# Kernel tuning notes

Hardware: AMD Instinct MI355X
Metric: run time of the kernel (lower is better)

Reference implementation:

```python
import jax, jax.numpy as jnp
import numpy as np
import math

# LLaMA-7B-style int8 attention (torch-int Int8LlamaAttention)
B, S, HID, NH, HD = 2, 1024, 4096, 32, 128
THETA = 10000.0
# per-tensor quantization scales (as produced by from_float)
S_IN, S_W, S_B = 0.02, 0.01, 0.1
S_Q, S_K, S_V, S_O = 0.05, 0.05, 0.05, 0.05


def _rope_tables(position_ids):
    inv_freq = 1.0 / (THETA ** (jnp.arange(0, HD, 2, dtype=jnp.float32) / HD))
    freqs = position_ids.astype(jnp.float32)[..., None] * inv_freq  # [B,S,HD//2]
    emb = jnp.concatenate([freqs, freqs], axis=-1)  # [B,S,HD]
    return jnp.cos(emb)[:, None], jnp.sin(emb)[:, None]  # [B,1,S,HD]


def _rotate_half(x):
    return jnp.concatenate([-x[..., HD // 2:], x[..., :HD // 2]], axis=-1)


def _quant_i8(x):
    return jnp.clip(jnp.round(x), -128, 127).astype(jnp.int8)


def _w8a8b8o8(x_i8, w_i8, b_i8, alpha, beta):
    # int8 GEMM with int32 accumulation, fused dequant-requant to int8
    acc = jnp.einsum('bsk,nk->bsn', x_i8.astype(jnp.int32), w_i8.astype(jnp.int32))
    return _quant_i8(acc.astype(jnp.float32) * alpha + b_i8.astype(jnp.float32) * beta)


def setup_inputs() -> dict:
    key = jax.random.key(0)
    ks = jax.random.split(key, 9)
    ri8 = lambda k, shp: jax.random.randint(k, shp, -127, 128, dtype=jnp.int8)
    return {
        'hidden_states': jax.random.normal(ks[0], (B, S, HID), jnp.float32),
        'position_ids': jnp.broadcast_to(jnp.arange(S, dtype=jnp.int32), (B, S)),
        'w_q': ri8(ks[1], (HID, HID)),
        'w_k': ri8(ks[2], (HID, HID)),
        'w_v': ri8(ks[3], (HID, HID)),
        'w_o': ri8(ks[4], (HID, HID)),
        'b_q': ri8(ks[5], (HID,)),
        'b_k': ri8(ks[6], (HID,)),
        'b_v': ri8(ks[7], (HID,)),
        'b_o': jax.random.normal(ks[8], (HID,), jnp.float32) * 0.01,
    }


def reference(hidden_states, position_ids, w_q, w_k, w_v, w_o, b_q, b_k, b_v, b_o):
    # quantize activations, run int8 q/k/v projections (W8A8B8O8Linear)
    x_i8 = _quant_i8(hidden_states / S_IN)
    q = _w8a8b8o8(x_i8, w_q, b_q, S_IN * S_W / S_Q, S_B / S_Q)
    k = _w8a8b8o8(x_i8, w_k, b_k, S_IN * S_W / S_K, S_B / S_K)
    v = _w8a8b8o8(x_i8, w_v, b_v, S_IN * S_W / S_V, S_B / S_V)
    to_heads = lambda t: t.reshape(B, S, NH, HD).transpose(0, 2, 1, 3)  # [B,NH,S,HD]
    q, k, v = to_heads(q), to_heads(k), to_heads(v)
    # RoPE applied on dequantized int8 values, requantized for the int8 qk bmm
    cos, sin = _rope_tables(position_ids)
    qf, kf = q.astype(jnp.float32), k.astype(jnp.float32)
    q_i8 = _quant_i8(qf * cos + _rotate_half(qf) * sin)
    k_i8 = _quant_i8(kf * cos + _rotate_half(kf) * sin)
    # BMM_S8T_S8N_F32T: int8 QK^T -> fp32 with scale s_q*s_k, then /sqrt(d)
    attn = jnp.einsum('bhsd,bhtd->bhst', q_i8.astype(jnp.int32), k_i8.astype(jnp.int32))
    attn = attn.astype(jnp.float32) * (S_Q * S_K) / math.sqrt(HD)
    # NOTE: source never applies the attention mask (`attn_weights = attn_weights`)
    p = jax.nn.softmax(attn, axis=-1)
    # probs quantized to int8 with scale 1/127 for BMM_S8T_S8N_S8T
    p_i8 = _quant_i8(p * 127.0)
    ctx = jnp.einsum('bhst,bhtd->bhsd', p_i8.astype(jnp.int32), v.astype(jnp.int32))
    ctx_i8 = _quant_i8(ctx.astype(jnp.float32) * ((1.0 / 127.0) * S_V / S_O))
    ctx_i8 = ctx_i8.transpose(0, 2, 1, 3).reshape(B, S, HID)
    # W8A8BFP32OFP32 o_proj: int8 GEMM, fp32 output + fp32 bias
    out = jnp.einsum('bsk,nk->bsn', ctx_i8.astype(jnp.int32), w_o.astype(jnp.int32))
    return out.astype(jnp.float32) * (S_O * S_W) + b_o
```

## Files before the change

kernel.cpp:

```cpp
#include <hip/hip_runtime.h>
#include <hip/hip_bf16.h>
#include <cstdint>
#include <cstddef>

typedef int v4i __attribute__((ext_vector_type(4)));

#define NH 32
#define HD 128
#define SEQ 1024
#define HID 4096
#define BB 2
#define BKB 128

__device__ __forceinline__ signed char quant_i8(float x) {
    float r = rintf(x);
    r = fminf(fmaxf(r, -128.0f), 127.0f);
    return (signed char)r;
}

#define GLOAD_LDS16(g, l) \
    __builtin_amdgcn_global_load_lds((const __attribute__((address_space(1))) void*)(g), \
                                     (__attribute__((address_space(3))) void*)(l), 16, 0, 0)

__global__ __launch_bounds__(256) void pack4_i8_kernel(
    const int* __restrict__ s0, const int* __restrict__ s1,
    const int* __restrict__ s2, const int* __restrict__ s3,
    signed char* __restrict__ d0, signed char* __restrict__ d1,
    signed char* __restrict__ d2, signed char* __restrict__ d3, int n4)
{
    int i = blockIdx.x * 256 + threadIdx.x;
    int which = i >> 22;
    int idx = i & ((1 << 22) - 1);
    const int* src = (which == 0) ? s0 : (which == 1) ? s1 : (which == 2) ? s2 : s3;
    signed char* dst = (which == 0) ? d0 : (which == 1) ? d1 : (which == 2) ? d2 : d3;
    int4 v = ((const int4*)src)[idx];
    char4 c;
    c.x = (signed char)v.x; c.y = (signed char)v.y;
    c.z = (signed char)v.z; c.w = (signed char)v.w;
    ((char4*)dst)[idx] = c;
}

__global__ __launch_bounds__(256) void quant_x_kernel(const float* __restrict__ src,
                                                      signed char* __restrict__ dst, int n4) {
    int i = blockIdx.x * 256 + threadIdx.x;
    if (i >= n4) return;
    float4 v = ((const float4*)src)[i];
    char4 c;
    c.x = quant_i8(v.x * 50.0f);
    c.y = quant_i8(v.y * 50.0f);
    c.z = quant_i8(v.z * 50.0f);
    c.w = quant_i8(v.w * 50.0f);
    ((char4*)dst)[i] = c;
}

template<bool F32OUT>
__device__ __forceinline__ void gemm_core_db(
    const signed char* __restrict__ A, const signed char* __restrict__ Bw,
    const void* __restrict__ bias, void* __restrict__ outp,
    int m0, int n0, int N, int K, float alpha, float beta)
{
    __shared__ __align__(16) signed char sA[2 * 128 * BKB];
    __shared__ __align__(16) signed char sB[2 * 128 * BKB];

    const int t    = threadIdx.x;
    const int w    = t >> 6;
    const int lane = t & 63;
    const int lm   = lane & 15;
    const int quad = lane >> 4;
    const int wm   = (w >> 1) * 64;
    const int wn   = (w & 1) * 64;

    int srow[4], skc[4];
    #pragma unroll
    for (int p = 0; p < 4; p++) {
        int si = t + 256 * p;
        int row = si >> 3;
        srow[p] = row;
        skc[p] = ((si & 7) - row) & 7;
    }

    v4i acc[4][4] = {};

    #pragma unroll
    for (int p = 0; p < 4; p++) {
        GLOAD_LDS16(A  + (size_t)(m0 + srow[p]) * K + skc[p] * 16, sA + t * 16 + p * 4096);
        GLOAD_LDS16(Bw + (size_t)(n0 + srow[p]) * K + skc[p] * 16, sB + t * 16 + p * 4096);
    }

    int buf = 0;
    for (int k0 = 0; k0 < K; k0 += BKB) {
        __syncthreads();

        if (k0 + BKB < K) {
            int nb = buf ^ 1;
            #pragma unroll
            for (int p = 0; p < 4; p++) {
                GLOAD_LDS16(A  + (size_t)(m0 + srow[p]) * K + k0 + BKB + skc[p] * 16,
                            sA + nb * 16384 + t * 16 + p * 4096);
                GLOAD_LDS16(Bw + (size_t)(n0 + srow[p]) * K + k0 + BKB + skc[p] * 16,
                            sB + nb * 16384 + t * 16 + p * 4096);
            }
        }

        const signed char* pA = sA + buf * 16384;
        const signed char* pB = sB + buf * 16384;
        #pragma unroll
        for (int ks = 0; ks < 2; ks++) {
            const int slot = (ks * 4 + quad + lm) & 7;
            v4i af[4], bf[4];
            #pragma unroll
            for (int i = 0; i < 4; i++) {
                int row = wm + 16 * i + lm;
                af[i] = *(const v4i*)(pA + row * BKB + slot * 16);
            }
            #pragma unroll
            for (int j = 0; j < 4; j++) {
                int row = wn + 16 * j + lm;
                bf[j] = *(const v4i*)(pB + row * BKB + slot * 16);
            }
            #pragma unroll
            for (int i = 0; i < 4; i++)
                #pragma unroll
                for (int j = 0; j < 4; j++)
                    acc[i][j] = __builtin_amdgcn_mfma_i32_16x16x64_i8(af[i], bf[j], acc[i][j], 0, 0, 0);
        }
        buf ^= 1;
    }

    const int orow = quad * 4;
    #pragma unroll
    for (int i = 0; i < 4; i++) {
        #pragma unroll
        for (int j = 0; j < 4; j++) {
            #pragma unroll
            for (int r = 0; r < 4; r++) {
                int row = m0 + wm + 16 * i + orow + r;
                int col = n0 + wn + 16 * j + lm;
                float v = (float)acc[i][j][r];
                if (F32OUT) {
                    ((float*)outp)[(size_t)row * N + col] = v * alpha + ((const float*)bias)[col];
                } else {
                    float q = v * alpha + (float)((const int*)bias)[col] * beta;
                    ((signed char*)outp)[(size_t)row * N + col] = quant_i8(q);
                }
            }
        }
    }
}

__global__ __launch_bounds__(256) void gemm_qkv(
    const signed char* __restrict__ x8,
    const signed char* __restrict__ wq, const signed char* __restrict__ wk,
    const signed char* __restrict__ wv,
    const int* __restrict__ bq, const int* __restrict__ bk, const int* __restrict__ bv,
    signed char* __restrict__ q8, signed char* __restrict__ k8, signed char* __restrict__ v8)
{
    const int id  = blockIdx.x + 96 * blockIdx.y;
    const int xcd = id & 7;
    const int j   = id >> 3;
    const int g   = j >> 6;
    const int r   = j & 63;
    const int nb  = xcd * 12 + g * 4 + (r & 3);
    const int m0  = (r >> 2) * 128;
    const int which = nb >> 5;
    const int n0  = (nb & 31) * 128;
    const signed char* Bw = (which == 0) ? wq : (which == 1) ? wk : wv;
    const int* bias = (which == 0) ? bq : (which == 1) ? bk : bv;
    signed char* outp = (which == 0) ? q8 : (which == 1) ? k8 : v8;
    gemm_core_db<false>(x8, Bw, bias, outp, m0, n0, HID, HID, 0.004f, 2.0f);
}

__global__ __launch_bounds__(256) void gemm_o(
    const signed char* __restrict__ c8, const signed char* __restrict__ wo,
    const float* __restrict__ bo, float* __restrict__ outp)
{
    const int id  = blockIdx.x + 32 * blockIdx.y;
    const int xcd = id & 7;
    const int j   = id >> 3;
    const int nb  = xcd * 4 + (j & 3);
    const int m0  = (j >> 2) * 128;
    gemm_core_db<true>(c8, wo, bo, outp, m0, nb * 128, HID, HID, 0.0005f, 0.0f);
}

__global__ __launch_bounds__(128) void rope_kernel(
    const int* __restrict__ pos_ids, signed char* __restrict__ q,
    signed char* __restrict__ k, const signed char* __restrict__ v,
    signed char* __restrict__ vt)
{
    const int bid = blockIdx.x;
    const int sg = bid & 127;
    const int h  = (bid >> 7) & (NH - 1);
    const int b  = bid >> 12;
    const int d  = threadIdx.x;
    const int s0 = sg * 8;
    const int bh = b * NH + h;

    float inv = expf(-(float)(2 * (d & 63)) * (9.210340371976184f / 128.0f));

    float qd[8], qp[8], kd[8], kp[8];
    signed char vd[8];
    int pos[8];
    size_t base[8];
    #pragma unroll
    for (int i = 0; i < 8; i++) {
        int s = s0 + i;
        base[i] = ((size_t)(b * SEQ + s) * NH + h) * (size_t)HD;
        pos[i] = pos_ids[b * SEQ + s];
        qd[i] = (float)q[base[i] + d];
        qp[i] = (float)q[base[i] + (d ^ 64)];
        kd[i] = (float)k[base[i] + d];
        kp[i] = (float)k[base[i] + (d ^ 64)];
        vd[i] = v[base[i] + d];
    }
    __syncthreads();

    union { signed char c[8]; int2 i2; } vu;
    #pragma unroll
    for (int i = 0; i < 8; i++) {
        float freq = (float)pos[i] * inv;
        float cs, sn;
        __sincosf(freq, &sn, &cs);
        float rotq = (d < 64) ? -qp[i] : qp[i];
        float rotk = (d < 64) ? -kp[i] : kp[i];
        q[base[i] + d] = quant_i8(qd[i] * cs + rotq * sn);
        k[base[i] + d] = quant_i8(kd[i] * cs + rotk * sn);
        vu.c[i] = vd[i];
    }
    *(int2*)(vt + ((size_t)(bh * HD + d)) * SEQ + s0) = vu.i2;
}

__global__ __launch_bounds__(256) void attn_kernel(
    const signed char* __restrict__ q, const signed char* __restrict__ k,
    const signed char* __restrict__ vt, signed char* __restrict__ ctx)
{
    __shared__ __align__(16) signed char p8[32 * 1040];
    __shared__ float red[128];

    const int w    = threadIdx.x >> 6;
    const int lane = threadIdx.x & 63;
    const int bid  = blockIdx.x;
    const int mt   = bid & 31;
    const int bh   = bid >> 5;
    const int b    = bh >> 5, h = bh & 31;
    const int m0   = mt * 32;
    const int lm   = lane & 15;
    const int quad = lane >> 4;

    const float SCALE = 0.0025f / 11.313708498984761f;
    const float LOG2E = 1.4426950408889634f;

    const signed char* qb_base = q + ((size_t)(b * SEQ + m0 + lm) * NH + h) * (size_t)HD + quad * 16;
    v4i qb0 = *(const v4i*)qb_base;
    v4i qb1 = *(const v4i*)(qb_base + 64);
    const signed char* qb_base2 = qb_base + (size_t)16 * NH * HD;
    v4i qb2 = *(const v4i*)qb_base2;
    v4i qb3 = *(const v4i*)(qb_base2 + 64);

    float vals0[16][4], vals1[16][4];
    #pragma unroll
    for (int j = 0; j < 16; j++) {
        int t0 = w * 256 + j * 16;
        const signed char* kb = k + ((size_t)(b * SEQ + t0 + lm) * NH + h) * (size_t)HD + quad * 16;
        v4i a0 = *(const v4i*)kb;
        v4i a1 = *(const v4i*)(kb + 64);
        v4i acc0 = {}, acc1 = {};
        __builtin_amdgcn_s_setprio(1);
        acc0 = __builtin_amdgcn_mfma_i32_16x16x64_i8(a0, qb0, acc0, 0, 0, 0);
        acc0 = __builtin_amdgcn_mfma_i32_16x16x64_i8(a1, qb1, acc0, 0, 0, 0);
        acc1 = __builtin_amdgcn_mfma_i32_16x16x64_i8(a0, qb2, acc1, 0, 0, 0);
        acc1 = __builtin_amdgcn_mfma_i32_16x16x64_i8(a1, qb3, acc1, 0, 0, 0);
        __builtin_amdgcn_s_setprio(0);
        #pragma unroll
        for (int r = 0; r < 4; r++) {
            vals0[j][r] = (float)acc0[r] * SCALE;
            vals1[j][r] = (float)acc1[r] * SCALE;
        }
    }

    float mx0 = vals0[0][0], mx1 = vals1[0][0];
    #pragma unroll
    for (int j = 0; j < 16; j++)
        #pragma unroll
        for (int r = 0; r < 4; r++) {
            mx0 = fmaxf(mx0, vals0[j][r]);
            mx1 = fmaxf(mx1, vals1[j][r]);
        }
    mx0 = fmaxf(mx0, __shfl_xor(mx0, 16)); mx0 = fmaxf(mx0, __shfl_xor(mx0, 32));
    mx1 = fmaxf(mx1, __shfl_xor(mx1, 16)); mx1 = fmaxf(mx1, __shfl_xor(mx1, 32));
    if (lane < 16) { red[w * 16 + lane] = mx0; red[64 + w * 16 + lane] = mx1; }
    __syncthreads();
    mx0 = fmaxf(fmaxf(red[lm], red[16 + lm]), fmaxf(red[32 + lm], red[48 + lm]));
    mx1 = fmaxf(fmaxf(red[64 + lm], red[80 + lm]), fmaxf(red[96 + lm], red[112 + lm]));

    float sum0 = 0.f, sum1 = 0.f;
    #pragma unroll
    for (int j = 0; j < 16; j++)
        #pragma unroll
        for (int r = 0; r < 4; r++) {
            vals0[j][r] = exp2f((vals0[j][r] - mx0) * LOG2E); sum0 += vals0[j][r];
            vals1[j][r] = exp2f((vals1[j][r] - mx1) * LOG2E); sum1 += vals1[j][r];
        }
    sum0 += __shfl_xor(sum0, 16); sum0 += __shfl_xor(sum0, 32);
    sum1 += __shfl_xor(sum1, 16); sum1 += __shfl_xor(sum1, 32);
    __syncthreads();
    if (lane < 16) { red[w * 16 + lane] = sum0; red[64 + w * 16 + lane] = sum1; }
    __syncthreads();
    sum0 = (red[lm] + red[16 + lm]) + (red[32 + lm] + red[48 + lm]);
    sum1 = (red[64 + lm] + red[80 + lm]) + (red[96 + lm] + red[112 + lm]);
    float sf0 = 127.0f / sum0, sf1 = 127.0f / sum1;

    #pragma unroll
    for (int j = 0; j < 16; j++) {
        union { signed char cc[4]; int ii; } u0, u1;
        #pragma unroll
        for (int r = 0; r < 4; r++) {
            u0.cc[r] = quant_i8(vals0[j][r] * sf0);
            u1.cc[r] = quant_i8(vals1[j][r] * sf1);
        }
        int ch = (((w * 16 + j) + 4 * lm) & 63) * 16 + quad * 4;
        *(int*)(p8 + lm * 1040 + ch) = u0.ii;
        *(int*)(p8 + (16 + lm) * 1040 + ch) = u1.ii;
    }
    __syncthreads();

    v4i accp0[2] = {}, accp1[2] = {};
    for (int kk = 0; kk < SEQ; kk += 64) {
        int ph = (((kk >> 4) + quad) + 4 * lm) & 63;
        v4i af0 = *(const v4i*)(p8 + lm * 1040 + ph * 16);
        v4i af1 = *(const v4i*)(p8 + (16 + lm) * 1040 + ph * 16);
        v4i vb0 = *(const v4i*)(vt + ((size_t)(bh * HD + w * 32 + lm)) * (size_t)SEQ + kk + quad * 16);
        v4i vb1 = *(const v4i*)(vt + ((size_t)(bh * HD + w * 32 + 16 + lm)) * (size_t)SEQ + kk + quad * 16);
        __builtin_amdgcn_s_setprio(1);
        accp0[0] = __builtin_amdgcn_mfma_i32_16x16x64_i8(af0, vb0, accp0[0], 0, 0, 0);
        accp1[0] = __builtin_amdgcn_mfma_i32_16x16x64_i8(af1, vb0, accp1[0], 0, 0, 0);
        accp0[1] = __builtin_amdgcn_mfma_i32_16x16x64_i8(af0, vb1, accp0[1], 0, 0, 0);
        accp1[1] = __builtin_amdgcn_mfma_i32_16x16x64_i8(af1, vb1, accp1[1], 0, 0, 0);
        __builtin_amdgcn_s_setprio(0);
    }
    #pragma unroll
    for (int j = 0; j < 2; j++) {
        #pragma unroll
        for (int r = 0; r < 4; r++) {
            int row = quad * 4 + r;
            int col = w * 32 + j * 16 + lm;
            ctx[((size_t)(b * SEQ + m0 + row) * NH + h) * (size_t)HD + col] =
                quant_i8((float)accp0[j][r] * (1.0f / 127.0f));
            ctx[((size_t)(b * SEQ + m0 + 16 + row) * NH + h) * (size_t)HD + col] =
                quant_i8((float)accp1[j][r] * (1.0f / 127.0f));
        }
    }
}

extern "C" void kernel_launch(void* const* d_in, const int* in_sizes, int n_in,
                              void* d_out, int out_size, void* d_ws, size_t ws_size,
                              hipStream_t stream)
{
    const float* hidden = (const float*)d_in[0];
    const int* pos_ids  = (const int*)d_in[1];
    const int* w_q = (const int*)d_in[2];
    const int* w_k = (const int*)d_in[3];
    const int* w_v = (const int*)d_in[4];
    const int* w_o = (const int*)d_in[5];
    const int* b_q = (const int*)d_in[6];
    const int* b_k = (const int*)d_in[7];
    const int* b_v = (const int*)d_in[8];
    const float* b_o = (const float*)d_in[9];
    float* out = (float*)d_out;

    char* ws = (char*)d_ws;
    const size_t WSZ = (size_t)HID * HID;
    signed char* wq8 = (signed char*)ws;
    signed char* wk8 = wq8 + WSZ;
    signed char* wv8 = wk8 + WSZ;
    signed char* wo8 = wv8 + WSZ;
    signed char* x8  = wo8 + WSZ;
    const size_t ASZ = (size_t)BB * SEQ * HID;
    signed char* q8  = x8 + ASZ;
    signed char* k8  = q8 + ASZ;
    signed char* v8  = k8 + ASZ;
    signed char* vt8 = v8 + ASZ;
    signed char* c8  = vt8 + ASZ;

    int wn4 = HID * HID / 4;
    pack4_i8_kernel<<<4 * wn4 / 256, 256, 0, stream>>>(w_q, w_k, w_v, w_o,
                                                       wq8, wk8, wv8, wo8, wn4);
    int xn4 = (int)(ASZ / 4);
    quant_x_kernel<<<xn4 / 256, 256, 0, stream>>>(hidden, x8, xn4);

    gemm_qkv<<<dim3(96, 16), 256, 0, stream>>>(x8, wq8, wk8, wv8, b_q, b_k, b_v,
                                               q8, k8, v8);

    rope_kernel<<<BB * NH * (SEQ / 8), 128, 0, stream>>>(pos_ids, q8, k8, v8, vt8);
    attn_kernel<<<BB * NH * (SEQ / 32), 256, 0, stream>>>(q8, k8, vt8, c8);

    gemm_o<<<dim3(32, 16), 256, 0, stream>>>(c8, wo8, b_o, out);
}
```

Measured before the change: 549.3 us.

## Rewrite int8 GEMMs with larger 512-thread tiles and 4-stage pipelined LDS loads

Replaces the double-buffered 128x128 int8 GEMM core with a templated kernel that uses 256-wide N tiles (256x256 for QKV, 128x256 for O), 512 threads and a 4-slot LDS ring with BK=64. Loads are prefetched two k-steps ahead, with explicit vmcnt waits, raw barriers and setprio around the MFMA bursts. The aim is better global-load/compute overlap and more data reuse per tile, at the cost of dropping the XCD-aware block swizzle and adding fragile hand-tuned wait counts.

Measured after the change: 558.6 us. About the same (+1.7%).

```diff
diff --git a/kernel.cpp b/kernel.cpp
--- a/kernel.cpp
+++ b/kernel.cpp
@@ -10,7 +10,6 @@
 #define SEQ 1024
 #define HID 4096
 #define BB 2
-#define BKB 128
 
 __device__ __forceinline__ signed char quant_i8(float x) {
     float r = rintf(x);
@@ -53,83 +52,110 @@
     ((char4*)dst)[i] = c;
 }
 
-template<bool F32OUT>
-__device__ __forceinline__ void gemm_core_db(
+template<int MFRAG, bool F32OUT>
+__device__ __forceinline__ void gemm8p(
     const signed char* __restrict__ A, const signed char* __restrict__ Bw,
     const void* __restrict__ bias, void* __restrict__ outp,
     int m0, int n0, int N, int K, float alpha, float beta)
 {
-    __shared__ __align__(16) signed char sA[2 * 128 * BKB];
-    __shared__ __align__(16) signed char sB[2 * 128 * BKB];
+    constexpr int BM = MFRAG * 32;
+    constexpr int BN = 256;
+    constexpr int LA = BM / 128;
+    constexpr int LB = BN / 128;
+    const int NKT = K >> 6;
+
+    __shared__ __align__(16) signed char sA[4][BM * 64];
+    __shared__ __align__(16) signed char sB[4][BN * 64];
 
     const int t    = threadIdx.x;
     const int w    = t >> 6;
     const int lane = t & 63;
     const int lm   = lane & 15;
     const int quad = lane >> 4;
-    const int wm   = (w >> 1) * 64;
-    const int wn   = (w & 1) * 64;
-
-    int srow[4], skc[4];
-    #pragma unroll
-    for (int p = 0; p < 4; p++) {
-        int si = t + 256 * p;
-        int row = si >> 3;
-        srow[p] = row;
-        skc[p] = ((si & 7) - row) & 7;
-    }
-
-    v4i acc[4][4] = {};
-
-    #pragma unroll
-    for (int p = 0; p < 4; p++) {
-        GLOAD_LDS16(A  + (size_t)(m0 + srow[p]) * K + skc[p] * 16, sA + t * 16 + p * 4096);
-        GLOAD_LDS16(Bw + (size_t)(n0 + srow[p]) * K + skc[p] * 16, sB + t * 16 + p * 4096);
-    }
-
-    int buf = 0;
-    for (int k0 = 0; k0 < K; k0 += BKB) {
-        __syncthreads();
-
-        if (k0 + BKB < K) {
-            int nb = buf ^ 1;
+    const int wm   = (w >> 2) * (BM / 2);
+    const int wn   = (w & 3) * 64;
+
+    v4i acc[MFRAG][4] = {};
+
+    auto stageA = [&](int kt) {
+        const signed char* src = A + (size_t)m0 * K + (kt << 6);
+        signed char* dst = &sA[kt & 3][0];
+        #pragma unroll
+        for (int p = 0; p < LA; p++) {
+            int si = p * 512 + t;
+            int row = si >> 2;
+            int c = ((si & 3) - (row >> 1)) & 3;
+            GLOAD_LDS16(src + (size_t)row * K + c * 16, dst + si * 16);
+        }
+    };
+    auto stageB = [&](int kt) {
+        const signed char* src = Bw + (size_t)n0 * K + (kt << 6);
+        signed char* dst = &sB[kt & 3][0];
+        #pragma unroll
+        for (int p = 0; p < LB; p++) {
+            int si = p * 512 + t;
+            int row = si >> 2;
+            int c = ((si & 3) - (row >> 1)) & 3;
+            GLOAD_LDS16(src + (size_t)row * K + c * 16, dst + si * 16);
+        }
+    };
+    auto rd = [&](const signed char* p, int rowl) -> v4i {
+        return *(const v4i*)(p + rowl * 64 + ((((rowl >> 1) + quad) & 3) << 4));
+    };
+
+    stageA(0); stageB(0);
+    stageA(1); stageB(1);
+    if constexpr (LA + LB == 4) asm volatile("s_waitcnt vmcnt(4)" ::: "memory");
+    else                        asm volatile("s_waitcnt vmcnt(3)" ::: "memory");
+    __builtin_amdgcn_s_barrier();
+
+    for (int kt = 0; kt < NKT; kt++) {
+        const signed char* pA = &sA[kt & 3][0];
+        const signed char* pB = &sB[kt & 3][0];
+        const bool pre = (kt + 2 < NKT);
+
+        v4i bf[4], af[4];
+        #pragma unroll
+        for (int j = 0; j < 4; j++) bf[j] = rd(pB, wn + 16 * j + lm);
+        #pragma unroll
+        for (int i = 0; i < 4; i++) af[i] = rd(pA, wm + 16 * i + lm);
+        if (pre) stageA(kt + 2);
+        if constexpr (MFRAG == 4) {
+            if (pre) stageB(kt + 2);
+            if (kt < NKT - 2)       asm volatile("s_waitcnt vmcnt(3)" ::: "memory");
+            else if (kt == NKT - 2) asm volatile("s_waitcnt vmcnt(0)" ::: "memory");
+        }
+        __builtin_amdgcn_s_barrier();
+        __builtin_amdgcn_s_setprio(1);
+        #pragma unroll
+        for (int i = 0; i < 4; i++)
             #pragma unroll
-            for (int p = 0; p < 4; p++) {
-                GLOAD_LDS16(A  + (size_t)(m0 + srow[p]) * K + k0 + BKB + skc[p] * 16,
-                            sA + nb * 16384 + t * 16 + p * 4096);
-                GLOAD_LDS16(Bw + (size_t)(n0 + srow[p]) * K + k0 + BKB + skc[p] * 16,
-                            sB + nb * 16384 + t * 16 + p * 4096);
-            }
-        }
-
-        const signed char* pA = sA + buf * 16384;
-        const signed char* pB = sB + buf * 16384;
-        #pragma unroll
-        for (int ks = 0; ks < 2; ks++) {
-            const int slot = (ks * 4 + quad + lm) & 7;
-            v4i af[4], bf[4];
+            for (int j = 0; j < 4; j++)
+                acc[i][j] = __builtin_amdgcn_mfma_i32_16x16x64_i8(af[i], bf[j], acc[i][j], 0, 0, 0);
+        __builtin_amdgcn_s_setprio(0);
+        __builtin_amdgcn_s_barrier();
+
+        if constexpr (MFRAG == 8) {
             #pragma unroll
-            for (int i = 0; i < 4; i++) {
-                int row = wm + 16 * i + lm;
-                af[i] = *(const v4i*)(pA + row * BKB + slot * 16);
-            }
-            #pragma unroll
-            for (int j = 0; j < 4; j++) {
-                int row = wn + 16 * j + lm;
-                bf[j] = *(const v4i*)(pB + row * BKB + slot * 16);
-            }
+            for (int i = 0; i < 4; i++) af[i] = rd(pA, wm + 64 + 16 * i + lm);
+            if (pre) stageB(kt + 2);
+            if (kt < NKT - 2)       asm volatile("s_waitcnt vmcnt(4)" ::: "memory");
+            else if (kt == NKT - 2) asm volatile("s_waitcnt vmcnt(0)" ::: "memory");
+            __builtin_amdgcn_s_barrier();
+            __builtin_amdgcn_s_setprio(1);
             #pragma unroll
             for (int i = 0; i < 4; i++)
                 #pragma unroll
                 for (int j = 0; j < 4; j++)
-                    acc[i][j] = __builtin_amdgcn_mfma_i32_16x16x64_i8(af[i], bf[j], acc[i][j], 0, 0, 0);
-        }
-        buf ^= 1;
+                    acc[4 + i][j] = __builtin_amdgcn_mfma_i32_16x16x64_i8(af[i], bf[j], acc[4 + i][j], 0, 0, 0);
+            __builtin_amdgcn_s_setprio(0);
+            __builtin_amdgcn_s_barrier();
+        }
     }
 
     const int orow = quad * 4;
     #pragma unroll
-    for (int i = 0; i < 4; i++) {
+    for (int i = 0; i < MFRAG; i++) {
         #pragma unroll
         for (int j = 0; j < 4; j++) {
             #pragma unroll
@@ -148,38 +174,31 @@
     }
 }
 
-__global__ __launch_bounds__(256) void gemm_qkv(
+__global__ __launch_bounds__(512, 2) void gemm_qkv(
     const signed char* __restrict__ x8,
     const signed char* __restrict__ wq, const signed char* __restrict__ wk,
     const signed char* __restrict__ wv,
     const int* __restrict__ bq, const int* __restrict__ bk, const int* __restrict__ bv,
     signed char* __restrict__ q8, signed char* __restrict__ k8, signed char* __restrict__ v8)
 {
-    const int id  = blockIdx.x + 96 * blockIdx.y;
-    const int xcd = id & 7;
-    const int j   = id >> 3;
-    const int g   = j >> 6;
-    const int r   = j & 63;
-    const int nb  = xcd * 12 + g * 4 + (r & 3);
-    const int m0  = (r >> 2) * 128;
-    const int which = nb >> 5;
-    const int n0  = (nb & 31) * 128;
+    const int id = blockIdx.x;
+    const int nb = id % 48;
+    const int mt = id / 48;
+    const int which = nb >> 4;
+    const int n0 = (nb & 15) * 256;
     const signed char* Bw = (which == 0) ? wq : (which == 1) ? wk : wv;
     const int* bias = (which == 0) ? bq : (which == 1) ? bk : bv;
     signed char* outp = (which == 0) ? q8 : (which == 1) ? k8 : v8;
-    gemm_core_db<false>(x8, Bw, bias, outp, m0, n0, HID, HID, 0.004f, 2.0f);
-}
-
-__global__ __launch_bounds__(256) void gemm_o(
+    gemm8p<8, false>(x8, Bw, bias, outp, mt * 256, n0, HID, HID, 0.004f, 2.0f);
+}
+
+__global__ __launch_bounds__(512, 2) void gemm_o(
     const signed char* __restrict__ c8, const signed char* __restrict__ wo,
     const float* __restrict__ bo, float* __restrict__ outp)
 {
-    const int id  = blockIdx.x + 32 * blockIdx.y;
-    const int xcd = id & 7;
-    const int j   = id >> 3;
-    const int nb  = xcd * 4 + (j & 3);
-    const int m0  = (j >> 2) * 128;
-    gemm_core_db<true>(c8, wo, bo, outp, m0, nb * 128, HID, HID, 0.0005f, 0.0f);
+    const int id = blockIdx.x;
+    gemm8p<4, true>(c8, wo, bo, outp, (id >> 4) * 128, (id & 15) * 256,
+                    HID, HID, 0.0005f, 0.0f);
 }
 
 __global__ __launch_bounds__(128) void rope_kernel(
@@ -387,11 +406,11 @@
     int xn4 = (int)(ASZ / 4);
     quant_x_kernel<<<xn4 / 256, 256, 0, stream>>>(hidden, x8, xn4);
 
-    gemm_qkv<<<dim3(96, 16), 256, 0, stream>>>(x8, wq8, wk8, wv8, b_q, b_k, b_v,
-                                               q8, k8, v8);
+    gemm_qkv<<<384, 512, 0, stream>>>(x8, wq8, wk8, wv8, b_q, b_k, b_v,
+                                      q8, k8, v8);
 
     rope_kernel<<<BB * NH * (SEQ / 8), 128, 0, stream>>>(pos_ids, q8, k8, v8, vt8);
     attn_kernel<<<BB * NH * (SEQ / 32), 256, 0, stream>>>(q8, k8, vt8, c8);
 
-    gemm_o<<<dim3(32, 16), 256, 0, stream>>>(c8, wo8, b_o, out);
-}
+    gemm_o<<<256, 512, 0, stream>>>(c8, wo8, b_o, out);
+}
```

## Prepack weights in MFMA fragment order and load B directly to registers

Applied to the files above, without the earlier changes.

The weight pack kernel now writes int8 weights in MFMA fragment order, so each lane can load its B fragment from global memory straight into registers without staging through LDS. The GEMM tile becomes 128x256 with BK=64, and only A goes through LDS with two buffers and explicit waitcnt/barrier pipelining plus setprio around the MFMA bursts. Grids are flattened with XCD-aware tile mapping and launch bounds ask for 2 blocks per CU. The aim is to cut LDS traffic and LDS usage for B and raise reuse per block, at the cost of more registers (32 accumulators) and reliance on hand-tuned vmcnt counts.

New measurement: 987.2 us. +79.7%, slower.

```diff
diff --git a/kernel.cpp b/kernel.cpp
--- a/kernel.cpp
+++ b/kernel.cpp
@@ -10,7 +10,6 @@
 #define SEQ 1024
 #define HID 4096
 #define BB 2
-#define BKB 128
 
 __device__ __forceinline__ signed char quant_i8(float x) {
     float r = rintf(x);
@@ -22,22 +21,32 @@
     __builtin_amdgcn_global_load_lds((const __attribute__((address_space(1))) void*)(g), \
                                      (__attribute__((address_space(3))) void*)(l), 16, 0, 0)
 
-__global__ __launch_bounds__(256) void pack4_i8_kernel(
+__global__ __launch_bounds__(256) void pack_frag_kernel(
     const int* __restrict__ s0, const int* __restrict__ s1,
     const int* __restrict__ s2, const int* __restrict__ s3,
     signed char* __restrict__ d0, signed char* __restrict__ d1,
-    signed char* __restrict__ d2, signed char* __restrict__ d3, int n4)
-{
-    int i = blockIdx.x * 256 + threadIdx.x;
-    int which = i >> 22;
-    int idx = i & ((1 << 22) - 1);
+    signed char* __restrict__ d2, signed char* __restrict__ d3)
+{
+    int g = blockIdx.x * 256 + threadIdx.x;
+    int which = g >> 20;
+    int u = g & 0xFFFFF;
+    int n  = u >> 8;
+    int kc = u & 255;
     const int* src = (which == 0) ? s0 : (which == 1) ? s1 : (which == 2) ? s2 : s3;
     signed char* dst = (which == 0) ? d0 : (which == 1) ? d1 : (which == 2) ? d2 : d3;
-    int4 v = ((const int4*)src)[idx];
-    char4 c;
-    c.x = (signed char)v.x; c.y = (signed char)v.y;
-    c.z = (signed char)v.z; c.w = (signed char)v.w;
-    ((char4*)dst)[idx] = c;
+
+    const int4* sp = (const int4*)(src + (size_t)n * HID + kc * 16);
+    union { signed char c[16]; int4 v; } out;
+    #pragma unroll
+    for (int q = 0; q < 4; q++) {
+        int4 v = sp[q];
+        out.c[4 * q + 0] = (signed char)v.x;
+        out.c[4 * q + 1] = (signed char)v.y;
+        out.c[4 * q + 2] = (signed char)v.z;
+        out.c[4 * q + 3] = (signed char)v.w;
+    }
+    int nf = n >> 4, kt = kc >> 2, ln = (kc & 3) * 16 + (n & 15);
+    ((int4*)dst)[(size_t)(nf * 64 + kt) * 64 + ln] = out.v;
 }
 
 __global__ __launch_bounds__(256) void quant_x_kernel(const float* __restrict__ src,
@@ -54,88 +63,108 @@
 }
 
 template<bool F32OUT>
-__device__ __forceinline__ void gemm_core_db(
-    const signed char* __restrict__ A, const signed char* __restrict__ Bw,
+__device__ __forceinline__ void gemm_dfb(
+    const signed char* __restrict__ A,
+    const signed char* __restrict__ Bp,
     const void* __restrict__ bias, void* __restrict__ outp,
     int m0, int n0, int N, int K, float alpha, float beta)
 {
-    __shared__ __align__(16) signed char sA[2 * 128 * BKB];
-    __shared__ __align__(16) signed char sB[2 * 128 * BKB];
+    __shared__ __align__(16) signed char sA0[128 * 64];
+    __shared__ __align__(16) signed char sA1[128 * 64];
 
     const int t    = threadIdx.x;
     const int w    = t >> 6;
     const int lane = t & 63;
     const int lm   = lane & 15;
     const int quad = lane >> 4;
-    const int wm   = (w >> 1) * 64;
-    const int wn   = (w & 1) * 64;
-
-    int srow[4], skc[4];
-    #pragma unroll
-    for (int p = 0; p < 4; p++) {
-        int si = t + 256 * p;
-        int row = si >> 3;
-        srow[p] = row;
-        skc[p] = ((si & 7) - row) & 7;
-    }
-
-    v4i acc[4][4] = {};
-
-    #pragma unroll
-    for (int p = 0; p < 4; p++) {
-        GLOAD_LDS16(A  + (size_t)(m0 + srow[p]) * K + skc[p] * 16, sA + t * 16 + p * 4096);
-        GLOAD_LDS16(Bw + (size_t)(n0 + srow[p]) * K + skc[p] * 16, sB + t * 16 + p * 4096);
-    }
-
-    int buf = 0;
-    for (int k0 = 0; k0 < K; k0 += BKB) {
-        __syncthreads();
-
-        if (k0 + BKB < K) {
-            int nb = buf ^ 1;
+    const int KT   = K >> 6;
+
+    const int r0 = t >> 2,          c0 = ((t & 3) - r0) & 3;
+    const int r1 = (t + 256) >> 2,  c1 = (((t + 256) & 3) - r1) & 3;
+    const signed char* aSrc0 = A + (size_t)(m0 + r0) * K + c0 * 16;
+    const signed char* aSrc1 = A + (size_t)(m0 + r1) * K + c1 * 16;
+
+    const size_t jstride = (size_t)KT * 1024;
+    const signed char* bBase = Bp + (size_t)((n0 >> 4) + w * 4) * jstride + (size_t)lane * 16;
+
+    v4i acc[8][4] = {};
+    v4i bfA[4], bfB[4], af[8];
+
+    auto stageA = [&](signed char* dst, int kt) {
+        GLOAD_LDS16(aSrc0 + kt * 64, dst + t * 16);
+        GLOAD_LDS16(aSrc1 + kt * 64, dst + (t + 256) * 16);
+    };
+    auto loadB = [&](v4i* bf, int kt) {
+        const signed char* p = bBase + (size_t)kt * 1024;
+        #pragma unroll
+        for (int j = 0; j < 4; j++) bf[j] = *(const v4i*)(p + (size_t)j * jstride);
+    };
+    auto rdA = [&](const signed char* slot) {
+        #pragma unroll
+        for (int i = 0; i < 8; i++) {
+            int r = 16 * i + lm;
+            af[i] = *(const v4i*)(slot + r * 64 + (((r + quad) & 3) << 4));
+        }
+    };
+
+    stageA(sA0, 0);
+    __builtin_amdgcn_sched_barrier(0);
+    loadB(bfA, 0);
+    asm volatile("s_waitcnt vmcnt(4)" ::: "memory");
+    __builtin_amdgcn_s_barrier();
+
+    for (int kt = 0; kt < KT; kt += 2) {
+        stageA(sA1, kt + 1);
+        __builtin_amdgcn_sched_barrier(0);
+        loadB(bfB, kt + 1);
+        __builtin_amdgcn_sched_barrier(0);
+        rdA(sA0);
+        __builtin_amdgcn_s_setprio(1);
+        #pragma unroll
+        for (int i = 0; i < 8; i++)
             #pragma unroll
-            for (int p = 0; p < 4; p++) {
-                GLOAD_LDS16(A  + (size_t)(m0 + srow[p]) * K + k0 + BKB + skc[p] * 16,
-                            sA + nb * 16384 + t * 16 + p * 4096);
-                GLOAD_LDS16(Bw + (size_t)(n0 + srow[p]) * K + k0 + BKB + skc[p] * 16,
-                            sB + nb * 16384 + t * 16 + p * 4096);
-            }
-        }
-
-        const signed char* pA = sA + buf * 16384;
-        const signed char* pB = sB + buf * 16384;
-        #pragma unroll
-        for (int ks = 0; ks < 2; ks++) {
-            const int slot = (ks * 4 + quad + lm) & 7;
-            v4i af[4], bf[4];
+            for (int j = 0; j < 4; j++)
+                acc[i][j] = __builtin_amdgcn_mfma_i32_16x16x64_i8(af[i], bfA[j], acc[i][j], 0, 0, 0);
+        __builtin_amdgcn_s_setprio(0);
+        asm volatile("s_waitcnt vmcnt(4)" ::: "memory");
+        __builtin_amdgcn_s_barrier();
+
+        if (kt + 2 < KT) {
+            stageA(sA0, kt + 2);
+            __builtin_amdgcn_sched_barrier(0);
+            loadB(bfA, kt + 2);
+            __builtin_amdgcn_sched_barrier(0);
+            rdA(sA1);
+            __builtin_amdgcn_s_setprio(1);
             #pragma unroll
-            for (int i = 0; i < 4; i++) {
-                int row = wm + 16 * i + lm;
-                af[i] = *(const v4i*)(pA + row * BKB + slot * 16);
-            }
-            #pragma unroll
-            for (int j = 0; j < 4; j++) {
-                int row = wn + 16 * j + lm;
-                bf[j] = *(const v4i*)(pB + row * BKB + slot * 16);
-            }
-            #pragma unroll
-            for (int i = 0; i < 4; i++)
+            for (int i = 0; i < 8; i++)
                 #pragma unroll
                 for (int j = 0; j < 4; j++)
-                    acc[i][j] = __builtin_amdgcn_mfma_i32_16x16x64_i8(af[i], bf[j], acc[i][j], 0, 0, 0);
-        }
-        buf ^= 1;
+                    acc[i][j] = __builtin_amdgcn_mfma_i32_16x16x64_i8(af[i], bfB[j], acc[i][j], 0, 0, 0);
+            __builtin_amdgcn_s_setprio(0);
+            asm volatile("s_waitcnt vmcnt(4)" ::: "memory");
+            __builtin_amdgcn_s_barrier();
+        } else {
+            rdA(sA1);
+            __builtin_amdgcn_s_setprio(1);
+            #pragma unroll
+            for (int i = 0; i < 8; i++)
+                #pragma unroll
+                for (int j = 0; j < 4; j++)
+                    acc[i][j] = __builtin_amdgcn_mfma_i32_16x16x64_i8(af[i], bfB[j], acc[i][j], 0, 0, 0);
+            __builtin_amdgcn_s_setprio(0);
+        }
     }
 
     const int orow = quad * 4;
     #pragma unroll
-    for (int i = 0; i < 4; i++) {
+    for (int i = 0; i < 8; i++) {
         #pragma unroll
         for (int j = 0; j < 4; j++) {
             #pragma unroll
             for (int r = 0; r < 4; r++) {
-                int row = m0 + wm + 16 * i + orow + r;
-                int col = n0 + wn + 16 * j + lm;
+                int row = m0 + 16 * i + orow + r;
+                int col = n0 + w * 64 + 16 * j + lm;
                 float v = (float)acc[i][j][r];
                 if (F32OUT) {
                     ((float*)outp)[(size_t)row * N + col] = v * alpha + ((const float*)bias)[col];
@@ -148,38 +177,36 @@
     }
 }
 
-__global__ __launch_bounds__(256) void gemm_qkv(
+__global__ __launch_bounds__(256, 2) void gemm_qkv(
     const signed char* __restrict__ x8,
     const signed char* __restrict__ wq, const signed char* __restrict__ wk,
     const signed char* __restrict__ wv,
     const int* __restrict__ bq, const int* __restrict__ bk, const int* __restrict__ bv,
     signed char* __restrict__ q8, signed char* __restrict__ k8, signed char* __restrict__ v8)
 {
-    const int id  = blockIdx.x + 96 * blockIdx.y;
+    const int id  = blockIdx.x;
     const int xcd = id & 7;
     const int j   = id >> 3;
-    const int g   = j >> 6;
-    const int r   = j & 63;
-    const int nb  = xcd * 12 + g * 4 + (r & 3);
-    const int m0  = (r >> 2) * 128;
-    const int which = nb >> 5;
-    const int n0  = (nb & 31) * 128;
+    const int nb  = xcd * 6 + (j >> 4);
+    const int mt  = j & 15;
+    const int which = nb >> 4;
+    const int n0  = (nb & 15) * 256;
     const signed char* Bw = (which == 0) ? wq : (which == 1) ? wk : wv;
     const int* bias = (which == 0) ? bq : (which == 1) ? bk : bv;
     signed char* outp = (which == 0) ? q8 : (which == 1) ? k8 : v8;
-    gemm_core_db<false>(x8, Bw, bias, outp, m0, n0, HID, HID, 0.004f, 2.0f);
-}
-
-__global__ __launch_bounds__(256) void gemm_o(
+    gemm_dfb<false>(x8, Bw, bias, outp, mt * 128, n0, HID, HID, 0.004f, 2.0f);
+}
+
+__global__ __launch_bounds__(256, 2) void gemm_o(
     const signed char* __restrict__ c8, const signed char* __restrict__ wo,
     const float* __restrict__ bo, float* __restrict__ outp)
 {
-    const int id  = blockIdx.x + 32 * blockIdx.y;
+    const int id  = blockIdx.x;
     const int xcd = id & 7;
     const int j   = id >> 3;
-    const int nb  = xcd * 4 + (j & 3);
-    const int m0  = (j >> 2) * 128;
-    gemm_core_db<true>(c8, wo, bo, outp, m0, nb * 128, HID, HID, 0.0005f, 0.0f);
+    const int nb  = xcd * 2 + (j >> 4);
+    const int mt  = j & 15;
+    gemm_dfb<true>(c8, wo, bo, outp, mt * 128, nb * 256, HID, HID, 0.0005f, 0.0f);
 }
 
 __global__ __launch_bounds__(128) void rope_kernel(
@@ -381,17 +408,16 @@
     signed char* vt8 = v8 + ASZ;
     signed char* c8  = vt8 + ASZ;
 
-    int wn4 = HID * HID / 4;
-    pack4_i8_kernel<<<4 * wn4 / 256, 256, 0, stream>>>(w_q, w_k, w_v, w_o,
-                                                       wq8, wk8, wv8, wo8, wn4);
+    pack_frag_kernel<<<4 * (1 << 20) / 256, 256, 0, stream>>>(w_q, w_k, w_v, w_o,
+                                                              wq8, wk8, wv8, wo8);
     int xn4 = (int)(ASZ / 4);
     quant_x_kernel<<<xn4 / 256, 256, 0, stream>>>(hidden, x8, xn4);
 
-    gemm_qkv<<<dim3(96, 16), 256, 0, stream>>>(x8, wq8, wk8, wv8, b_q, b_k, b_v,
-                                               q8, k8, v8);
+    gemm_qkv<<<768, 256, 0, stream>>>(x8, wq8, wk8, wv8, b_q, b_k, b_v,
+                                      q8, k8, v8);
 
     rope_kernel<<<BB * NH * (SEQ / 8), 128, 0, stream>>>(pos_ids, q8, k8, v8, vt8);
     attn_kernel<<<BB * NH * (SEQ / 32), 256, 0, stream>>>(q8, k8, vt8, c8);
 
-    gemm_o<<<dim3(32, 16), 256, 0, stream>>>(c8, wo8, b_o, out);
-}
+    gemm_o<<<256, 256, 0, stream>>>(c8, wo8, b_o, out);
+}
```

## Halve GEMM K-tile to 64, raise occupancy, add MFMA priority, drop XCD remap

Applied to the files above, without the earlier changes.

The int8 GEMM core now uses a 64-byte K tile instead of 128, which halves LDS use per block (32KB instead of 64KB) and uses a new 4-slot swizzle. Launch bounds now request 4 blocks per CU. s_setprio is raised around the MFMA block. The XCD-aware block index remapping for L2 locality in both the QKV and O GEMMs is replaced by plain grid indexing. Higher occupancy should hide latency better, at the cost of twice as many barriers per K step and possibly worse L2 reuse across XCDs.

New measurement: 549.0 us. No clear change (-0.1%).

```diff
diff --git a/kernel.cpp b/kernel.cpp
--- a/kernel.cpp
+++ b/kernel.cpp
@@ -10,7 +10,6 @@
 #define SEQ 1024
 #define HID 4096
 #define BB 2
-#define BKB 128
 
 __device__ __forceinline__ signed char quant_i8(float x) {
     float r = rintf(x);
@@ -54,13 +53,13 @@
 }
 
 template<bool F32OUT>
-__device__ __forceinline__ void gemm_core_db(
+__device__ __forceinline__ void gemm128(
     const signed char* __restrict__ A, const signed char* __restrict__ Bw,
     const void* __restrict__ bias, void* __restrict__ outp,
     int m0, int n0, int N, int K, float alpha, float beta)
 {
-    __shared__ __align__(16) signed char sA[2 * 128 * BKB];
-    __shared__ __align__(16) signed char sB[2 * 128 * BKB];
+    __shared__ __align__(16) signed char sA[2][128 * 64];
+    __shared__ __align__(16) signed char sB[2][128 * 64];
 
     const int t    = threadIdx.x;
     const int w    = t >> 6;
@@ -70,60 +69,47 @@
     const int wm   = (w >> 1) * 64;
     const int wn   = (w & 1) * 64;
 
-    int srow[4], skc[4];
-    #pragma unroll
-    for (int p = 0; p < 4; p++) {
-        int si = t + 256 * p;
-        int row = si >> 3;
-        srow[p] = row;
-        skc[p] = ((si & 7) - row) & 7;
-    }
+    int row0 = t >> 2,          cc0 = ((t & 3) - (row0 >> 1)) & 3;
+    int row1 = (t + 256) >> 2,  cc1 = (((t + 256) & 3) - (row1 >> 1)) & 3;
+    const signed char* aS0 = A  + (size_t)(m0 + row0) * K + cc0 * 16;
+    const signed char* aS1 = A  + (size_t)(m0 + row1) * K + cc1 * 16;
+    const signed char* bS0 = Bw + (size_t)(n0 + row0) * K + cc0 * 16;
+    const signed char* bS1 = Bw + (size_t)(n0 + row1) * K + cc1 * 16;
 
     v4i acc[4][4] = {};
 
-    #pragma unroll
-    for (int p = 0; p < 4; p++) {
-        GLOAD_LDS16(A  + (size_t)(m0 + srow[p]) * K + skc[p] * 16, sA + t * 16 + p * 4096);
-        GLOAD_LDS16(Bw + (size_t)(n0 + srow[p]) * K + skc[p] * 16, sB + t * 16 + p * 4096);
-    }
+    GLOAD_LDS16(aS0, &sA[0][t * 16]);
+    GLOAD_LDS16(aS1, &sA[0][(t + 256) * 16]);
+    GLOAD_LDS16(bS0, &sB[0][t * 16]);
+    GLOAD_LDS16(bS1, &sB[0][(t + 256) * 16]);
+
+    const int aslot = ((quad + (wm >> 1) + (lm >> 1)) & 3) << 4;
+    const int bslot = ((quad + (wn >> 1) + (lm >> 1)) & 3) << 4;
 
     int buf = 0;
-    for (int k0 = 0; k0 < K; k0 += BKB) {
+    for (int k0 = 0; k0 < K; k0 += 64) {
         __syncthreads();
-
-        if (k0 + BKB < K) {
+        if (k0 + 64 < K) {
             int nb = buf ^ 1;
+            GLOAD_LDS16(aS0 + k0 + 64, &sA[nb][t * 16]);
+            GLOAD_LDS16(aS1 + k0 + 64, &sA[nb][(t + 256) * 16]);
+            GLOAD_LDS16(bS0 + k0 + 64, &sB[nb][t * 16]);
+            GLOAD_LDS16(bS1 + k0 + 64, &sB[nb][(t + 256) * 16]);
+        }
+        v4i af[4], bf[4];
+        #pragma unroll
+        for (int i = 0; i < 4; i++)
+            af[i] = *(const v4i*)(&sA[buf][(wm + 16 * i + lm) * 64 + aslot]);
+        #pragma unroll
+        for (int j = 0; j < 4; j++)
+            bf[j] = *(const v4i*)(&sB[buf][(wn + 16 * j + lm) * 64 + bslot]);
+        __builtin_amdgcn_s_setprio(1);
+        #pragma unroll
+        for (int i = 0; i < 4; i++)
             #pragma unroll
-            for (int p = 0; p < 4; p++) {
-                GLOAD_LDS16(A  + (size_t)(m0 + srow[p]) * K + k0 + BKB + skc[p] * 16,
-                            sA + nb * 16384 + t * 16 + p * 4096);
-                GLOAD_LDS16(Bw + (size_t)(n0 + srow[p]) * K + k0 + BKB + skc[p] * 16,
-                            sB + nb * 16384 + t * 16 + p * 4096);
-            }
-        }
-
-        const signed char* pA = sA + buf * 16384;
-        const signed char* pB = sB + buf * 16384;
-        #pragma unroll
-        for (int ks = 0; ks < 2; ks++) {
-            const int slot = (ks * 4 + quad + lm) & 7;
-            v4i af[4], bf[4];
-            #pragma unroll
-            for (int i = 0; i < 4; i++) {
-                int row = wm + 16 * i + lm;
-                af[i] = *(const v4i*)(pA + row * BKB + slot * 16);
-            }
-            #pragma unroll
-            for (int j = 0; j < 4; j++) {
-                int row = wn + 16 * j + lm;
-                bf[j] = *(const v4i*)(pB + row * BKB + slot * 16);
-            }
-            #pragma unroll
-            for (int i = 0; i < 4; i++)
-                #pragma unroll
-                for (int j = 0; j < 4; j++)
-                    acc[i][j] = __builtin_amdgcn_mfma_i32_16x16x64_i8(af[i], bf[j], acc[i][j], 0, 0, 0);
-        }
+            for (int j = 0; j < 4; j++)
+                acc[i][j] = __builtin_amdgcn_mfma_i32_16x16x64_i8(af[i], bf[j], acc[i][j], 0, 0, 0);
+        __builtin_amdgcn_s_setprio(0);
         buf ^= 1;
     }
 
@@ -148,38 +134,29 @@
     }
 }
 
-__global__ __launch_bounds__(256) void gemm_qkv(
+__global__ __launch_bounds__(256, 4) void gemm_qkv(
     const signed char* __restrict__ x8,
     const signed char* __restrict__ wq, const signed char* __restrict__ wk,
     const signed char* __restrict__ wv,
     const int* __restrict__ bq, const int* __restrict__ bk, const int* __restrict__ bv,
     signed char* __restrict__ q8, signed char* __restrict__ k8, signed char* __restrict__ v8)
 {
-    const int id  = blockIdx.x + 96 * blockIdx.y;
-    const int xcd = id & 7;
-    const int j   = id >> 3;
-    const int g   = j >> 6;
-    const int r   = j & 63;
-    const int nb  = xcd * 12 + g * 4 + (r & 3);
-    const int m0  = (r >> 2) * 128;
-    const int which = nb >> 5;
-    const int n0  = (nb & 31) * 128;
+    const int nblk = blockIdx.x;
+    const int which = nblk >> 5;
+    const int n0 = (nblk & 31) * 128;
+    const int m0 = blockIdx.y * 128;
     const signed char* Bw = (which == 0) ? wq : (which == 1) ? wk : wv;
     const int* bias = (which == 0) ? bq : (which == 1) ? bk : bv;
     signed char* outp = (which == 0) ? q8 : (which == 1) ? k8 : v8;
-    gemm_core_db<false>(x8, Bw, bias, outp, m0, n0, HID, HID, 0.004f, 2.0f);
-}
-
-__global__ __launch_bounds__(256) void gemm_o(
+    gemm128<false>(x8, Bw, bias, outp, m0, n0, HID, HID, 0.004f, 2.0f);
+}
+
+__global__ __launch_bounds__(256, 4) void gemm_o(
     const signed char* __restrict__ c8, const signed char* __restrict__ wo,
     const float* __restrict__ bo, float* __restrict__ outp)
 {
-    const int id  = blockIdx.x + 32 * blockIdx.y;
-    const int xcd = id & 7;
-    const int j   = id >> 3;
-    const int nb  = xcd * 4 + (j & 3);
-    const int m0  = (j >> 2) * 128;
-    gemm_core_db<true>(c8, wo, bo, outp, m0, nb * 128, HID, HID, 0.0005f, 0.0f);
+    gemm128<true>(c8, wo, bo, outp, blockIdx.y * 128, blockIdx.x * 128,
+                  HID, HID, 0.0005f, 0.0f);
 }
 
 __global__ __launch_bounds__(128) void rope_kernel(
```
